# Kernel tuning notes

Measured on AMD Instinct MI355X. Metric: run time of the kernel, lower is better.

## Reference

```python
import jax, jax.numpy as jnp
import numpy as np

NUM_CLASSES = 20
STRIDE = 32
INPUT_SIZE = 2560
CONF_THRESH = 0.01
NMS_THRESH = 0.5
G = INPUT_SIZE // STRIDE          # 80 grid cells per side
N = G * G                         # 6400 candidate boxes
EPS = 1e-28                       # epsilon from original pure-python NMS


def _make_grid():
    # torch.meshgrid default 'ij' indexing: flat index n = x*G + y, entry [x, y]
    gx, gy = jnp.meshgrid(jnp.arange(G, dtype=jnp.float32),
                          jnp.arange(G, dtype=jnp.float32), indexing='ij')
    return jnp.stack([gx, gy], axis=-1).reshape(N, 2)


def _decode_boxes(txtytwth):
    # (grid + sigmoid(txty)) * stride -> center; exp(twth) -> width/height
    cxcy = (_make_grid() + jax.nn.sigmoid(txtytwth[:, :2])) * STRIDE
    wh = jnp.exp(txtytwth[:, 2:])
    boxes = jnp.concatenate([cxcy - wh * 0.5, cxcy + wh * 0.5], axis=-1)
    return jnp.clip(boxes / INPUT_SIZE, 0.0, 1.0)  # [N,4] xyxy in [0,1]


def _batched_nms(boxes, scores, class_idx):
    """Per-class greedy NMS via class-offset trick (equivalent to looping classes)."""
    # translate each class's boxes to a disjoint region so cross-class IoU ~ 0
    b = boxes + class_idx.astype(boxes.dtype)[:, None] * 2.0
    order = jnp.argsort(-scores)              # descending score order
    b = b[order]
    areas = (b[:, 2] - b[:, 0]) * (b[:, 3] - b[:, 1])
    xx1 = jnp.maximum(b[:, None, 0], b[None, :, 0])
    yy1 = jnp.maximum(b[:, None, 1], b[None, :, 1])
    xx2 = jnp.minimum(b[:, None, 2], b[None, :, 2])
    yy2 = jnp.minimum(b[:, None, 3], b[None, :, 3])
    w = jnp.maximum(EPS, xx2 - xx1)
    h = jnp.maximum(EPS, yy2 - yy1)
    inter = w * h                             # [N,N] pairwise intersection
    iou = inter / (areas[:, None] + areas[None, :] - inter)
    valid = scores[order] >= CONF_THRESH      # conf filter before NMS
    idxs = jnp.arange(N)

    def body(i, keep):
        supp = (iou[i] > NMS_THRESH) & (idxs > i)
        return jnp.where(keep[i], keep & ~supp, keep)

    keep_sorted = jax.lax.fori_loop(0, N, body, valid)
    return jnp.zeros(N, dtype=bool).at[order].set(keep_sorted)


def reference(pred):
    p = pred[0]                                   # inference path uses batch 0 only
    conf = jax.nn.sigmoid(p[:, :1])               # objectness
    cls_scores = jax.nn.softmax(p[:, 1:1 + NUM_CLASSES], axis=1) * conf
    boxes = _decode_boxes(p[:, 1 + NUM_CLASSES:])
    class_idx = jnp.argmax(cls_scores, axis=1)
    scores = jnp.max(cls_scores, axis=1)
    keep = _batched_nms(boxes, scores, class_idx)
    # fixed-shape outputs: non-kept detections have score zeroed, keep mask returned
    return boxes, scores * keep, class_idx.astype(jnp.int32), keep


def setup_inputs() -> dict:
    key = jax.random.key(0)
    pred = jax.random.normal(key, (1, N, 1 + NUM_CLASSES + 4), dtype=jnp.float32)
    return {"pred": pred}
```

## Files before the change

### kernel.cpp

```cpp
#include <hip/hip_runtime.h>
#include <stdint.h>

#define NBOX 6400
#define GRIDW 80
#define NC 20
#define NBLK 100

__device__ __forceinline__ float sigmoidf(float x) { return 1.0f / (1.0f + expf(-x)); }

__device__ __forceinline__ void decode_one(const float* __restrict__ p, int n,
        float4* box, float* score, int* cls) {
    float conf = sigmoidf(p[0]);
    float c[NC];
    float m = -INFINITY;
    #pragma unroll
    for (int j = 0; j < NC; j++) { c[j] = p[1 + j]; m = fmaxf(m, c[j]); }
    float sum = 0.f;
    #pragma unroll
    for (int j = 0; j < NC; j++) { c[j] = expf(c[j] - m); sum += c[j]; }
    float best = -INFINITY; int bi = 0;
    #pragma unroll
    for (int j = 0; j < NC; j++) {
        float s = (c[j] / sum) * conf;
        if (s > best) { best = s; bi = j; }
    }
    float gx = (float)(n / GRIDW);
    float gy = (float)(n % GRIDW);
    float cx = (gx + sigmoidf(p[21])) * 32.0f;
    float cy = (gy + sigmoidf(p[22])) * 32.0f;
    float w = expf(p[23]);
    float h = expf(p[24]);
    box->x = fminf(fmaxf((cx - w * 0.5f) / 2560.0f, 0.0f), 1.0f);
    box->y = fminf(fmaxf((cy - h * 0.5f) / 2560.0f, 0.0f), 1.0f);
    box->z = fminf(fmaxf((cx + w * 0.5f) / 2560.0f, 0.0f), 1.0f);
    box->w = fminf(fmaxf((cy + h * 0.5f) / 2560.0f, 0.0f), 1.0f);
    *score = best;
    *cls = bi;
}

__global__ __launch_bounds__(256) void k_decode(const float* __restrict__ pred,
        float* __restrict__ out, float4* __restrict__ boff,
        float* __restrict__ score_ws, float4* __restrict__ blkbb,
        uint64_t* __restrict__ validw, uint32_t* __restrict__ flag,
        uint32_t* __restrict__ done) {
    int t = threadIdx.x;
    int n = blockIdx.x * 256 + t;
    int l = t & 63;
    if (n == 0) { flag[0] = 0u; done[0] = 0u; }
    float4 bx; float s; int cls;
    decode_one(pred + (size_t)n * 25, n, &bx, &s, &cls);
    ((float4*)out)[n] = bx;
    out[32000 + n] = (float)cls;
    bool valid = s >= 0.01f;
    out[25600 + n] = valid ? s : 0.0f;
    out[38400 + n] = valid ? 1.0f : 0.0f;
    score_ws[n] = s;
    float off = 2.0f * (float)cls;
    boff[n] = make_float4(bx.x + off, bx.y + off, bx.z + off, bx.w + off);

    float x1 = valid ? bx.x :  INFINITY;
    float y1 = valid ? bx.y :  INFINITY;
    float x2 = valid ? bx.z : -INFINITY;
    float y2 = valid ? bx.w : -INFINITY;
    #pragma unroll
    for (int d = 1; d < 64; d <<= 1) {
        x1 = fminf(x1, __shfl_xor(x1, d));
        y1 = fminf(y1, __shfl_xor(y1, d));
        x2 = fmaxf(x2, __shfl_xor(x2, d));
        y2 = fmaxf(y2, __shfl_xor(y2, d));
    }
    uint64_t vb = __ballot(valid);
    if (l == 0) {
        blkbb[n >> 6] = make_float4(x1, y1, x2, y2);
        validw[n >> 6] = vb;
    }
}

__global__ __launch_bounds__(256) void k_pairs(const float4* __restrict__ boff,
        const float4* __restrict__ blkbb, const uint64_t* __restrict__ validw,
        const float* __restrict__ score, uint32_t* __restrict__ flag,
        uint32_t* __restrict__ done, int* __restrict__ sidx,
        float* __restrict__ sscore, float4* __restrict__ sbox,
        float* __restrict__ out) {
    __shared__ float4 cblds[64];
    __shared__ uint64_t klds[NBOX];
    __shared__ uint32_t keepb[NBOX / 32];
    __shared__ uint32_t lastf;
    int t = threadIdx.x;
    int w = t >> 6, l = t & 63;
    int bi = blockIdx.x;

    float4 ra = blkbb[bi];
    uint64_t rowvalid = validw[bi];
    const float M = 1e-5f;
    uint64_t surv_lo = 0ull, surv_hi = 0ull;
    if (rowvalid != 0ull) {
        bool ov = false;
        int bj = bi + l;
        if (bj < NBLK) {
            float4 ca = blkbb[bj];
            ov = (fminf(ra.z, ca.z) + M >= fmaxf(ra.x, ca.x)) &&
                 (fminf(ra.w, ca.w) + M >= fmaxf(ra.y, ca.y));
        }
        surv_lo = __ballot(ov);
        ov = false;
        bj = bi + 64 + l;
        if (bj < NBLK) {
            float4 ca = blkbb[bj];
            ov = (fminf(ra.z, ca.z) + M >= fmaxf(ra.x, ca.x)) &&
                 (fminf(ra.w, ca.w) + M >= fmaxf(ra.y, ca.y));
        }
        surv_hi = __ballot(ov);
    }

    int i = bi * 64 + l;
    float4 rb = boff[i];
    float areai = (rb.z - rb.x) * (rb.w - rb.y);
    bool rv = (rowvalid >> l) & 1ull;
    bool hit = false;
    while ((surv_lo | surv_hi) != 0ull) {
        int d;
        if (surv_lo) { d = __ffsll((unsigned long long)surv_lo) - 1; surv_lo &= surv_lo - 1; }
        else { d = 64 + __ffsll((unsigned long long)surv_hi) - 1; surv_hi &= surv_hi - 1; }
        int bj = bi + d;
        uint64_t colvalid = validw[bj];
        __syncthreads();
        if (t < 64) cblds[t] = boff[bj * 64 + t];
        __syncthreads();
        if (colvalid != 0ull) {
            #pragma unroll
            for (int k2 = 0; k2 < 16; k2++) {
                int s2 = w * 16 + k2;
                float4 b = cblds[s2];
                bool ok = rv && ((colvalid >> s2) & 1ull) &&
                          !(bi == bj && s2 <= l);
                float xx1 = fmaxf(rb.x, b.x);
                float yy1 = fmaxf(rb.y, b.y);
                float xx2 = fminf(rb.z, b.z);
                float yy2 = fminf(rb.w, b.w);
                float ww = fmaxf(1e-28f, xx2 - xx1);
                float hh = fmaxf(1e-28f, yy2 - yy1);
                float inter = ww * hh;
                float areaj = (b.z - b.x) * (b.w - b.y);
                hit |= ok && (3.0f * inter >= 0.9995f * (areai + areaj));
            }
        }
    }
    if (__ballot(hit) != 0ull && l == 0) atomicOr(flag, 1u);

    __syncthreads();
    __threadfence();
    if (t == 0) lastf = (atomicAdd(done, 1u) == NBLK - 1) ? 1u : 0u;
    __syncthreads();
    if (!lastf) return;
    if (t == 0) lastf = atomicOr(flag, 0u);
    __syncthreads();
    if (!lastf) return;

    for (int n = t; n < NBOX; n += 256)
        klds[n] = (((uint64_t)(~__float_as_uint(score[n]))) << 32) | (uint32_t)n;
    __syncthreads();
    for (int n = t; n < NBOX; n += 256) {
        uint64_t mk = klds[n];
        int r = 0;
        for (int j = 0; j < NBOX; j++) r += (klds[j] < mk) ? 1 : 0;
        sidx[r] = n;
        sscore[r] = score[n];
        sbox[r] = boff[n];
    }
    __syncthreads();
    for (int w2 = t; w2 < NBOX / 32; w2 += 256) {
        uint32_t v = 0;
        for (int b = 0; b < 32; b++) v |= (sscore[w2 * 32 + b] >= 0.01f) ? (1u << b) : 0u;
        keepb[w2] = v;
    }
    __syncthreads();
    for (int ii = 0; ii < NBOX; ii++) {
        bool kept = (keepb[ii >> 5] >> (ii & 31)) & 1u;
        if (kept) {
            float4 a = sbox[ii];
            float areaa = (a.z - a.x) * (a.w - a.y);
            for (int j = ii + 1 + t; j < NBOX; j += 256) {
                if ((keepb[j >> 5] >> (j & 31)) & 1u) {
                    float4 b = sbox[j];
                    float xx1 = fmaxf(a.x, b.x);
                    float yy1 = fmaxf(a.y, b.y);
                    float xx2 = fminf(a.z, b.z);
                    float yy2 = fminf(a.w, b.w);
                    float ww = fmaxf(1e-28f, xx2 - xx1);
                    float hh = fmaxf(1e-28f, yy2 - yy1);
                    float inter = ww * hh;
                    float areab = (b.z - b.x) * (b.w - b.y);
                    float iou = inter / (areaa + areab - inter);
                    if (iou > 0.5f) atomicAnd(&keepb[j >> 5], ~(1u << (j & 31)));
                }
            }
        }
        __syncthreads();
    }
    for (int r = t; r < NBOX; r += 256) {
        int orig = sidx[r];
        uint32_t kb = (keepb[r >> 5] >> (r & 31)) & 1u;
        out[38400 + orig] = (float)kb;
        out[25600 + orig] = kb ? sscore[r] : 0.0f;
    }
}

extern "C" void kernel_launch(void* const* d_in, const int* in_sizes, int n_in,
                              void* d_out, int out_size, void* d_ws, size_t ws_size,
                              hipStream_t stream) {
    const float* pred = (const float*)d_in[0];
    float* out = (float*)d_out;
    char* ws = (char*)d_ws;
    float4*   boff   = (float4*)(ws + 0);
    float*    score  = (float*)(ws + 102400);
    float4*   blkbb  = (float4*)(ws + 128000);
    uint64_t* validw = (uint64_t*)(ws + 129600);
    uint32_t* flag   = (uint32_t*)(ws + 130432);
    uint32_t* done   = (uint32_t*)(ws + 130436);
    int*      sidx   = (int*)(ws + 131072);
    float*    sscore = (float*)(ws + 156672);
    float4*   sbox   = (float4*)(ws + 182272);

    k_decode<<<25, 256, 0, stream>>>(pred, out, boff, score, blkbb, validw, flag, done);
    k_pairs<<<NBLK, 256, 0, stream>>>(boff, blkbb, validw, score, flag, done,
                                      sidx, sscore, sbox, out);
}
```

Measured before the change: 66.17 us.

## Fuse decode and overlap check into one kernel with redundant neighbor decoding

Merges the decode and pairwise pre-check kernels into one launch. Each block recomputes the boxes of its own 64-box chunk plus the next eight chunks in shared memory and tests all pairs against a fixed window. Any valid box wider than a threshold forces the exact path, which keeps the bounded window safe. The last block polls per-block ready flags instead of counting with an atomic, and runs the exact sorted NMS only when a potential suppression was found. This removes a kernel launch and the global bounding-box pass in exchange for extra decode work. The ready flags use a constant magic value that is never reset, so a later call could see stale flags.

```diff
diff --git a/kernel.cpp b/kernel.cpp
--- a/kernel.cpp
+++ b/kernel.cpp
@@ -5,11 +5,14 @@
 #define GRIDW 80
 #define NC 20
 #define NBLK 100
+#define NCH 9
+#define WMAX_PX 160.0f
+#define MAGIC 0x13579BDFu
 
 __device__ __forceinline__ float sigmoidf(float x) { return 1.0f / (1.0f + expf(-x)); }
 
 __device__ __forceinline__ void decode_one(const float* __restrict__ p, int n,
-        float4* box, float* score, int* cls) {
+        float4* box, float* score, int* cls, float* raww) {
     float conf = sigmoidf(p[0]);
     float c[NC];
     float m = -INFINITY;
@@ -36,142 +39,121 @@
     box->w = fminf(fmaxf((cy + h * 0.5f) / 2560.0f, 0.0f), 1.0f);
     *score = best;
     *cls = bi;
+    *raww = w;
 }
 
-__global__ __launch_bounds__(256) void k_decode(const float* __restrict__ pred,
+__global__ __launch_bounds__(256) void k_all(const float* __restrict__ pred,
         float* __restrict__ out, float4* __restrict__ boff,
-        float* __restrict__ score_ws, float4* __restrict__ blkbb,
-        uint64_t* __restrict__ validw, uint32_t* __restrict__ flag,
-        uint32_t* __restrict__ done) {
-    int t = threadIdx.x;
-    int n = blockIdx.x * 256 + t;
-    int l = t & 63;
-    if (n == 0) { flag[0] = 0u; done[0] = 0u; }
-    float4 bx; float s; int cls;
-    decode_one(pred + (size_t)n * 25, n, &bx, &s, &cls);
-    ((float4*)out)[n] = bx;
-    out[32000 + n] = (float)cls;
-    bool valid = s >= 0.01f;
-    out[25600 + n] = valid ? s : 0.0f;
-    out[38400 + n] = valid ? 1.0f : 0.0f;
-    score_ws[n] = s;
-    float off = 2.0f * (float)cls;
-    boff[n] = make_float4(bx.x + off, bx.y + off, bx.z + off, bx.w + off);
-
-    float x1 = valid ? bx.x :  INFINITY;
-    float y1 = valid ? bx.y :  INFINITY;
-    float x2 = valid ? bx.z : -INFINITY;
-    float y2 = valid ? bx.w : -INFINITY;
-    #pragma unroll
-    for (int d = 1; d < 64; d <<= 1) {
-        x1 = fminf(x1, __shfl_xor(x1, d));
-        y1 = fminf(y1, __shfl_xor(y1, d));
-        x2 = fmaxf(x2, __shfl_xor(x2, d));
-        y2 = fmaxf(y2, __shfl_xor(y2, d));
-    }
-    uint64_t vb = __ballot(valid);
-    if (l == 0) {
-        blkbb[n >> 6] = make_float4(x1, y1, x2, y2);
-        validw[n >> 6] = vb;
-    }
-}
-
-__global__ __launch_bounds__(256) void k_pairs(const float4* __restrict__ boff,
-        const float4* __restrict__ blkbb, const uint64_t* __restrict__ validw,
-        const float* __restrict__ score, uint32_t* __restrict__ flag,
-        uint32_t* __restrict__ done, int* __restrict__ sidx,
-        float* __restrict__ sscore, float4* __restrict__ sbox,
-        float* __restrict__ out) {
-    __shared__ float4 cblds[64];
+        float* __restrict__ score_g, uint32_t* __restrict__ hitw,
+        uint32_t* __restrict__ ready, int* __restrict__ sidx,
+        float* __restrict__ sscore, float4* __restrict__ sbox) {
+    __shared__ float4 bl[NCH * 64];
     __shared__ uint64_t klds[NBOX];
     __shared__ uint32_t keepb[NBOX / 32];
-    __shared__ uint32_t lastf;
+    __shared__ uint32_t whit[4];
+    __shared__ uint32_t sh_flag;
     int t = threadIdx.x;
     int w = t >> 6, l = t & 63;
-    int bi = blockIdx.x;
-
-    float4 ra = blkbb[bi];
-    uint64_t rowvalid = validw[bi];
-    const float M = 1e-5f;
-    uint64_t surv_lo = 0ull, surv_hi = 0ull;
-    if (rowvalid != 0ull) {
-        bool ov = false;
-        int bj = bi + l;
-        if (bj < NBLK) {
-            float4 ca = blkbb[bj];
-            ov = (fminf(ra.z, ca.z) + M >= fmaxf(ra.x, ca.x)) &&
-                 (fminf(ra.w, ca.w) + M >= fmaxf(ra.y, ca.y));
-        }
-        surv_lo = __ballot(ov);
-        ov = false;
-        bj = bi + 64 + l;
-        if (bj < NBLK) {
-            float4 ca = blkbb[bj];
-            ov = (fminf(ra.z, ca.z) + M >= fmaxf(ra.x, ca.x)) &&
-                 (fminf(ra.w, ca.w) + M >= fmaxf(ra.y, ca.y));
-        }
-        surv_hi = __ballot(ov);
-    }
-
-    int i = bi * 64 + l;
-    float4 rb = boff[i];
+    int b = blockIdx.x;
+    int nreal = (NBLK - b) < NCH ? (NBLK - b) * 64 : NCH * 64;
+
+    bool bigbox = false;
+    for (int m = t; m < NCH * 64; m += 256) {
+        float4 ob;
+        if (m < nreal) {
+            int n = b * 64 + m;
+            float4 bx; float s; int cls; float rw;
+            decode_one(pred + (size_t)n * 25, n, &bx, &s, &cls, &rw);
+            bool valid = s >= 0.01f;
+            float off = 2.0f * (float)cls;
+            float4 tob = make_float4(bx.x + off, bx.y + off, bx.z + off, bx.w + off);
+            if (m < 64) {
+                ((float4*)out)[n] = bx;
+                out[32000 + n] = (float)cls;
+                out[25600 + n] = valid ? s : 0.0f;
+                out[38400 + n] = valid ? 1.0f : 0.0f;
+                score_g[n] = s;
+                boff[n] = tob;
+                bigbox |= valid && (rw > WMAX_PX);
+            }
+            if (valid) ob = tob;
+            else { float fx = -10000.0f - (float)m;
+                   ob = make_float4(fx, 0.0f, fx + 0.5f, 0.5f); }
+        } else {
+            float fx = -10000.0f - (float)m;
+            ob = make_float4(fx, 0.0f, fx + 0.5f, 0.5f);
+        }
+        bl[m] = ob;
+    }
+    __syncthreads();
+
+    float4 rb = bl[l];
     float areai = (rb.z - rb.x) * (rb.w - rb.y);
-    bool rv = (rowvalid >> l) & 1ull;
-    bool hit = false;
-    while ((surv_lo | surv_hi) != 0ull) {
-        int d;
-        if (surv_lo) { d = __ffsll((unsigned long long)surv_lo) - 1; surv_lo &= surv_lo - 1; }
-        else { d = 64 + __ffsll((unsigned long long)surv_hi) - 1; surv_hi &= surv_hi - 1; }
-        int bj = bi + d;
-        uint64_t colvalid = validw[bj];
-        __syncthreads();
-        if (t < 64) cblds[t] = boff[bj * 64 + t];
-        __syncthreads();
-        if (colvalid != 0ull) {
-            #pragma unroll
-            for (int k2 = 0; k2 < 16; k2++) {
-                int s2 = w * 16 + k2;
-                float4 b = cblds[s2];
-                bool ok = rv && ((colvalid >> s2) & 1ull) &&
-                          !(bi == bj && s2 <= l);
-                float xx1 = fmaxf(rb.x, b.x);
-                float yy1 = fmaxf(rb.y, b.y);
-                float xx2 = fminf(rb.z, b.z);
-                float yy2 = fminf(rb.w, b.w);
-                float ww = fmaxf(1e-28f, xx2 - xx1);
-                float hh = fmaxf(1e-28f, yy2 - yy1);
-                float inter = ww * hh;
-                float areaj = (b.z - b.x) * (b.w - b.y);
-                hit |= ok && (3.0f * inter >= 0.9995f * (areai + areaj));
-            }
-        }
-    }
-    if (__ballot(hit) != 0ull && l == 0) atomicOr(flag, 1u);
-
+    bool hit = bigbox;
+    #pragma unroll
+    for (int c = 0; c < NCH; c++) {
+        #pragma unroll
+        for (int k2 = 0; k2 < 16; k2++) {
+            int s2 = w * 16 + k2;
+            float4 bb = bl[c * 64 + s2];
+            bool ok = !(c == 0 && s2 <= l);
+            float xx1 = fmaxf(rb.x, bb.x);
+            float yy1 = fmaxf(rb.y, bb.y);
+            float xx2 = fminf(rb.z, bb.z);
+            float yy2 = fminf(rb.w, bb.w);
+            float ww = fmaxf(1e-28f, xx2 - xx1);
+            float hh = fmaxf(1e-28f, yy2 - yy1);
+            float inter = ww * hh;
+            float areaj = (bb.z - bb.x) * (bb.w - bb.y);
+            hit |= ok && (3.0f * inter >= 0.9995f * (areai + areaj));
+        }
+    }
+    whit[w] = (__ballot(hit) != 0ull) ? 1u : 0u;
+    __syncthreads();
+    if (t == 0) {
+        hitw[b] = whit[0] | whit[1] | whit[2] | whit[3];
+        __threadfence();
+        __hip_atomic_store(&ready[b], MAGIC, __ATOMIC_RELEASE, __HIP_MEMORY_SCOPE_AGENT);
+    }
+    if (b != NBLK - 1) return;
+
+    if (t < 64) {
+        bool need0 = (t < NBLK), need1 = (t + 64 < NBLK);
+        for (;;) {
+            bool ok = (!need0 || __hip_atomic_load(&ready[t], __ATOMIC_RELAXED,
+                                     __HIP_MEMORY_SCOPE_AGENT) == MAGIC)
+                   && (!need1 || __hip_atomic_load(&ready[t + 64], __ATOMIC_RELAXED,
+                                     __HIP_MEMORY_SCOPE_AGENT) == MAGIC);
+            if (__ballot(ok) == ~0ull) break;
+            __builtin_amdgcn_s_sleep(2);
+        }
+    }
     __syncthreads();
     __threadfence();
-    if (t == 0) lastf = (atomicAdd(done, 1u) == NBLK - 1) ? 1u : 0u;
-    __syncthreads();
-    if (!lastf) return;
-    if (t == 0) lastf = atomicOr(flag, 0u);
-    __syncthreads();
-    if (!lastf) return;
+    if (t < 64) {
+        uint32_t h = (t < NBLK ? hitw[t] : 0u) | (t + 64 < NBLK ? hitw[t + 64] : 0u);
+        uint64_t anyb = __ballot(h == 1u);
+        if (t == 0) sh_flag = (anyb != 0ull) ? 1u : 0u;
+    }
+    __syncthreads();
+    if (sh_flag != 1u) return;
 
     for (int n = t; n < NBOX; n += 256)
-        klds[n] = (((uint64_t)(~__float_as_uint(score[n]))) << 32) | (uint32_t)n;
+        klds[n] = (((uint64_t)(~__float_as_uint(score_g[n]))) << 32) | (uint32_t)n;
     __syncthreads();
     for (int n = t; n < NBOX; n += 256) {
         uint64_t mk = klds[n];
         int r = 0;
         for (int j = 0; j < NBOX; j++) r += (klds[j] < mk) ? 1 : 0;
         sidx[r] = n;
-        sscore[r] = score[n];
+        sscore[r] = score_g[n];
         sbox[r] = boff[n];
     }
     __syncthreads();
     for (int w2 = t; w2 < NBOX / 32; w2 += 256) {
         uint32_t v = 0;
-        for (int b = 0; b < 32; b++) v |= (sscore[w2 * 32 + b] >= 0.01f) ? (1u << b) : 0u;
+        for (int bb2 = 0; bb2 < 32; bb2++)
+            v |= (sscore[w2 * 32 + bb2] >= 0.01f) ? (1u << bb2) : 0u;
         keepb[w2] = v;
     }
     __syncthreads();
@@ -182,15 +164,15 @@
             float areaa = (a.z - a.x) * (a.w - a.y);
             for (int j = ii + 1 + t; j < NBOX; j += 256) {
                 if ((keepb[j >> 5] >> (j & 31)) & 1u) {
-                    float4 b = sbox[j];
-                    float xx1 = fmaxf(a.x, b.x);
-                    float yy1 = fmaxf(a.y, b.y);
-                    float xx2 = fminf(a.z, b.z);
-                    float yy2 = fminf(a.w, b.w);
+                    float4 bb = sbox[j];
+                    float xx1 = fmaxf(a.x, bb.x);
+                    float yy1 = fmaxf(a.y, bb.y);
+                    float xx2 = fminf(a.z, bb.z);
+                    float yy2 = fminf(a.w, bb.w);
                     float ww = fmaxf(1e-28f, xx2 - xx1);
                     float hh = fmaxf(1e-28f, yy2 - yy1);
                     float inter = ww * hh;
-                    float areab = (b.z - b.x) * (b.w - b.y);
+                    float areab = (bb.z - bb.x) * (bb.w - bb.y);
                     float iou = inter / (areaa + areab - inter);
                     if (iou > 0.5f) atomicAnd(&keepb[j >> 5], ~(1u << (j & 31)));
                 }
@@ -214,15 +196,12 @@
     char* ws = (char*)d_ws;
     float4*   boff   = (float4*)(ws + 0);
     float*    score  = (float*)(ws + 102400);
-    float4*   blkbb  = (float4*)(ws + 128000);
-    uint64_t* validw = (uint64_t*)(ws + 129600);
-    uint32_t* flag   = (uint32_t*)(ws + 130432);
-    uint32_t* done   = (uint32_t*)(ws + 130436);
-    int*      sidx   = (int*)(ws + 131072);
-    float*    sscore = (float*)(ws + 156672);
-    float4*   sbox   = (float4*)(ws + 182272);
-
-    k_decode<<<25, 256, 0, stream>>>(pred, out, boff, score, blkbb, validw, flag, done);
-    k_pairs<<<NBLK, 256, 0, stream>>>(boff, blkbb, validw, score, flag, done,
-                                      sidx, sscore, sbox, out);
+    uint32_t* hitw   = (uint32_t*)(ws + 128000);
+    uint32_t* ready  = (uint32_t*)(ws + 128512);
+    int*      sidx   = (int*)(ws + 129024);
+    float*    sscore = (float*)(ws + 154624);
+    float4*   sbox   = (float4*)(ws + 180224);
+
+    k_all<<<NBLK, 256, 0, stream>>>(pred, out, boff, score, hitw, ready,
+                                    sidx, sscore, sbox);
 }
```

After: 68.62 us. 3.7% more time.
